# Performance work log

Measured on AMD Instinct MI355X. Metric: run time of the kernel, lower is better.

Reference implementation:

```python
import jax, jax.numpy as jnp
import numpy as np

NUM_STEPS = 151


def setup_inputs() -> dict:
    key = jax.random.key(0)
    k1, k2 = jax.random.split(key)
    feats = jax.random.normal(k1, (1024, 128), dtype=jnp.float32)
    # dists must lie in [-1, 1] -> L2-normalize embeddings (cosine similarity)
    feats = feats / jnp.linalg.norm(feats, axis=1, keepdims=True)
    classes = jax.random.randint(k2, (1024,), 0, 100, dtype=jnp.int32)
    return {"features": feats, "classes": classes}


def reference(features, classes):
    n = features.shape[0]
    step = 2.0 / (NUM_STEPS - 1)
    # bin centers t_j = -1 + j*step, j = 0..NUM_STEPS-1 (torch.range(-1, 1, step))
    t = (-1.0 + jnp.arange(NUM_STEPS, dtype=jnp.float32) * step)[:, None]  # [T,1]

    dists = features @ features.T                      # [N,N]
    iu = jnp.triu_indices(n, k=1)                      # strict upper triangle
    s = dists[iu]                                      # [P] pairwise similarities
    eq = (classes[:, None] == classes[None, :])[iu]    # [P] same-class mask

    pos_size = jnp.sum(eq).astype(jnp.float32)
    neg_size = jnp.sum(~eq).astype(jnp.float32)

    # snap each similarity to the bin edge below it (detached, like .data in torch)
    delta = jnp.floor((jax.lax.stop_gradient(s) + 1.0) / step) * step - 1.0  # [P]

    indsa = delta[None, :] == (t - step)   # s falls in [t-step, t): rising edge
    indsb = delta[None, :] == t            # s falls in [t, t+step): falling edge
    wa = (s[None, :] - t + step) / step
    wb = (-s[None, :] + t + step) / step
    w = jnp.where(indsa, wa, jnp.where(indsb, wb, 0.0))  # [T,P] triangular weights

    hist_pos = jnp.sum(jnp.where(eq[None, :], w, 0.0), axis=1) / pos_size  # [T]
    hist_neg = jnp.sum(jnp.where(eq[None, :], 0.0, w), axis=1) / neg_size  # [T]

    # tril(ones,-1) zeroing + sum over dim 0 == inclusive cumulative sum
    hist_pos_cdf = jnp.cumsum(hist_pos)
    loss = jnp.sum(hist_neg * hist_pos_cdf)
    return loss
```

## Files before the change

### kernel.cpp

```cpp
#include <hip/hip_runtime.h>

#define T_STEPS 151
#define NN 1024
#define DD 128
#define TILE 32
#define NTILE (NN / TILE)
#define NBLOCKS (NTILE * (NTILE + 1) / 2)
#define LDSTRIDE 132
#define NPAIRS 523776.0f


__global__ __launch_bounds__(256) void hist_kernel(
    const float* __restrict__ F, const int* __restrict__ cls, float* __restrict__ ws)
{
    __shared__ float As[TILE][LDSTRIDE];
    __shared__ float Bs[TILE][LDSTRIDE];
    __shared__ float hpos[T_STEPS];
    __shared__ float hneg[T_STEPS];
    __shared__ int   clsA[TILE];
    __shared__ int   clsB[TILE];
    __shared__ float pcount;

    const int t = threadIdx.x;

    int rem = blockIdx.x;
    int bi = 0;
    while (rem >= (NTILE - bi)) { rem -= (NTILE - bi); ++bi; }
    const int bj = bi + rem;

    for (int k = t; k < T_STEPS; k += 256) { hpos[k] = 0.f; hneg[k] = 0.f; }
    if (t == 0) pcount = 0.f;
    if (t < TILE)            clsA[t]        = cls[bi * TILE + t];
    else if (t < 2 * TILE)   clsB[t - TILE] = cls[bj * TILE + (t - TILE)];

    const float* Abase = F + (size_t)bi * TILE * DD;
    const float* Bbase = F + (size_t)bj * TILE * DD;
    for (int idx = t; idx < TILE * DD / 4; idx += 256) {
        int r = idx >> 5;
        int c = (idx & 31) << 2;
        *(float4*)&As[r][c] = *(const float4*)(Abase + r * DD + c);
        *(float4*)&Bs[r][c] = *(const float4*)(Bbase + r * DD + c);
    }
    __syncthreads();

    const int r  = t >> 5;
    const int c  = t & 31;
    const int gj = bj * TILE + c;
    const int cb = clsB[c];

    float acc[4][4];
    #pragma unroll
    for (int p = 0; p < 4; ++p)
        #pragma unroll
        for (int q = 0; q < 4; ++q) acc[p][q] = 0.f;

    #pragma unroll 4
    for (int k = 0; k < DD; k += 4) {
        float4 b4 = *(const float4*)&Bs[c][k];
        #pragma unroll
        for (int p = 0; p < 4; ++p) {
            float4 a4 = *(const float4*)&As[r + 8 * p][k];
            acc[p][0] += a4.x * b4.x;
            acc[p][1] += a4.y * b4.y;
            acc[p][2] += a4.z * b4.z;
            acc[p][3] += a4.w * b4.w;
        }
    }

    const float STEP = 2.0f / 150.0f;
    float myp = 0.f;
    {
        #pragma clang fp contract(off)
        #pragma unroll
        for (int p = 0; p < 4; ++p) {
            int i  = r + 8 * p;
            int gi = bi * TILE + i;
            if (gi < gj) {
                float s = (acc[p][0] + acc[p][1]) + (acc[p][2] + acc[p][3]);
                bool eqf = (clsA[i] == cb);
                float kf    = floorf((s + 1.0f) / STEP);
                float delta = kf * STEP - 1.0f;
                int   kk    = (int)kf;
                if (kk >= 0 && kk < T_STEPS) {
                    float tk = -1.0f + (float)kk * STEP;
                    if (delta == tk) {
                        float wb = (-s + tk + STEP) / STEP;
                        atomicAdd(eqf ? &hpos[kk] : &hneg[kk], wb);
                    }
                }
                int k1 = kk + 1;
                if (k1 >= 0 && k1 < T_STEPS) {
                    float tk1 = -1.0f + (float)k1 * STEP;
                    if (delta == (tk1 - STEP)) {
                        float wa = (s - tk1 + STEP) / STEP;
                        atomicAdd(eqf ? &hpos[k1] : &hneg[k1], wa);
                    }
                }
                if (eqf) myp += 1.f;
            }
        }
    }
    atomicAdd(&pcount, myp);
    __syncthreads();

    for (int k = t; k < T_STEPS; k += 256) {
        float hp = hpos[k], hn = hneg[k];
        if (hp != 0.f) atomicAdd(&ws[k], hp);
        if (hn != 0.f) atomicAdd(&ws[T_STEPS + k], hn);
    }
    if (t == 0) atomicAdd(&ws[2 * T_STEPS], pcount);
}

__global__ __launch_bounds__(192) void final_kernel(
    const float* __restrict__ ws, float* __restrict__ out)
{
    __shared__ float hp[T_STEPS], hn[T_STEPS];
    int t = threadIdx.x;
    float pos = ws[2 * T_STEPS];
    float neg = NPAIRS - pos;
    if (t < T_STEPS) {
        hp[t] = ws[t] / pos;
        hn[t] = ws[T_STEPS + t] / neg;
    }
    __syncthreads();
    if (t == 0) {
        #pragma clang fp contract(off)
        float cdf = 0.f, loss = 0.f;
        for (int j = 0; j < T_STEPS; ++j) { cdf += hp[j]; loss += hn[j] * cdf; }
        *out = loss;
    }
}

extern "C" void kernel_launch(void* const* d_in, const int* in_sizes, int n_in,
                              void* d_out, int out_size, void* d_ws, size_t ws_size,
                              hipStream_t stream)
{
    const float* F   = (const float*)d_in[0];
    const int*   cls = (const int*)d_in[1];
    float*       ws  = (float*)d_ws;
    float*       out = (float*)d_out;

    hipMemsetAsync(d_ws, 0, (2 * T_STEPS + 1) * sizeof(float), stream);
    hist_kernel<<<NBLOCKS, 256, 0, stream>>>(F, cls, ws);
    final_kernel<<<1, 192, 0, stream>>>(ws, out);
}
```

Before: 86.14 us.

## Use 2x2 register tiling and per-block partial histograms instead of global atomics

The dot-product loop changes from a 4x1 to a 2x2 register tile per thread, so each thread loads two A and two B float4 rows per k step and gets more reuse per LDS load. Each block now writes its full partial histogram and positive count to its own workspace row instead of doing global atomics. The final kernel reduces all 528 rows with 1024 threads, which also removes the memset launch. In exchange the final kernel reads about 640 KB of partials serially from one block, which may cost more than the global atomics did.

```diff
diff --git a/kernel.cpp b/kernel.cpp
--- a/kernel.cpp
+++ b/kernel.cpp
@@ -7,6 +7,7 @@
 #define NTILE (NN / TILE)
 #define NBLOCKS (NTILE * (NTILE + 1) / 2)
 #define LDSTRIDE 132
+#define WSROW 304
 #define NPAIRS 523776.0f
 
 
@@ -43,28 +44,31 @@
     }
     __syncthreads();
 
-    const int r  = t >> 5;
-    const int c  = t & 31;
-    const int gj = bj * TILE + c;
-    const int cb = clsB[c];
+    const int r2 = t >> 4;
+    const int c2 = t & 15;
 
-    float acc[4][4];
+    float acc[2][2][4];
     #pragma unroll
-    for (int p = 0; p < 4; ++p)
+    for (int a = 0; a < 2; ++a)
         #pragma unroll
-        for (int q = 0; q < 4; ++q) acc[p][q] = 0.f;
+        for (int b = 0; b < 2; ++b)
+            #pragma unroll
+            for (int q = 0; q < 4; ++q) acc[a][b][q] = 0.f;
 
     #pragma unroll 4
     for (int k = 0; k < DD; k += 4) {
-        float4 b4 = *(const float4*)&Bs[c][k];
-        #pragma unroll
-        for (int p = 0; p < 4; ++p) {
-            float4 a4 = *(const float4*)&As[r + 8 * p][k];
-            acc[p][0] += a4.x * b4.x;
-            acc[p][1] += a4.y * b4.y;
-            acc[p][2] += a4.z * b4.z;
-            acc[p][3] += a4.w * b4.w;
-        }
+        float4 a0 = *(const float4*)&As[r2][k];
+        float4 a1 = *(const float4*)&As[r2 + 16][k];
+        float4 b0 = *(const float4*)&Bs[c2][k];
+        float4 b1 = *(const float4*)&Bs[c2 + 16][k];
+        acc[0][0][0] += a0.x * b0.x; acc[0][0][1] += a0.y * b0.y;
+        acc[0][0][2] += a0.z * b0.z; acc[0][0][3] += a0.w * b0.w;
+        acc[0][1][0] += a0.x * b1.x; acc[0][1][1] += a0.y * b1.y;
+        acc[0][1][2] += a0.z * b1.z; acc[0][1][3] += a0.w * b1.w;
+        acc[1][0][0] += a1.x * b0.x; acc[1][0][1] += a1.y * b0.y;
+        acc[1][0][2] += a1.z * b0.z; acc[1][0][3] += a1.w * b0.w;
+        acc[1][1][0] += a1.x * b1.x; acc[1][1][1] += a1.y * b1.y;
+        acc[1][1][2] += a1.z * b1.z; acc[1][1][3] += a1.w * b1.w;
     }
 
     const float STEP = 2.0f / 150.0f;
@@ -72,61 +76,83 @@
     {
         #pragma clang fp contract(off)
         #pragma unroll
-        for (int p = 0; p < 4; ++p) {
-            int i  = r + 8 * p;
-            int gi = bi * TILE + i;
-            if (gi < gj) {
-                float s = (acc[p][0] + acc[p][1]) + (acc[p][2] + acc[p][3]);
-                bool eqf = (clsA[i] == cb);
-                float kf    = floorf((s + 1.0f) / STEP);
-                float delta = kf * STEP - 1.0f;
-                int   kk    = (int)kf;
-                if (kk >= 0 && kk < T_STEPS) {
-                    float tk = -1.0f + (float)kk * STEP;
-                    if (delta == tk) {
-                        float wb = (-s + tk + STEP) / STEP;
-                        atomicAdd(eqf ? &hpos[kk] : &hneg[kk], wb);
+        for (int ii = 0; ii < 2; ++ii) {
+            #pragma unroll
+            for (int jj = 0; jj < 2; ++jj) {
+                int gi = bi * TILE + r2 + 16 * ii;
+                int gj = bj * TILE + c2 + 16 * jj;
+                if (gi < gj) {
+                    float* a = acc[ii][jj];
+                    float s = (a[0] + a[1]) + (a[2] + a[3]);
+                    bool eqf = (clsA[r2 + 16 * ii] == clsB[c2 + 16 * jj]);
+                    float kf    = floorf((s + 1.0f) / STEP);
+                    float delta = kf * STEP - 1.0f;
+                    int   kk    = (int)kf;
+                    if (kk >= 0 && kk < T_STEPS) {
+                        float tk = -1.0f + (float)kk * STEP;
+                        if (delta == tk) {
+                            float wb = (-s + tk + STEP) / STEP;
+                            atomicAdd(eqf ? &hpos[kk] : &hneg[kk], wb);
+                        }
                     }
+                    int k1 = kk + 1;
+                    if (k1 >= 0 && k1 < T_STEPS) {
+                        float tk1 = -1.0f + (float)k1 * STEP;
+                        if (delta == (tk1 - STEP)) {
+                            float wa = (s - tk1 + STEP) / STEP;
+                            atomicAdd(eqf ? &hpos[k1] : &hneg[k1], wa);
+                        }
+                    }
+                    if (eqf) myp += 1.f;
                 }
-                int k1 = kk + 1;
-                if (k1 >= 0 && k1 < T_STEPS) {
-                    float tk1 = -1.0f + (float)k1 * STEP;
-                    if (delta == (tk1 - STEP)) {
-                        float wa = (s - tk1 + STEP) / STEP;
-                        atomicAdd(eqf ? &hpos[k1] : &hneg[k1], wa);
-                    }
-                }
-                if (eqf) myp += 1.f;
             }
         }
     }
     atomicAdd(&pcount, myp);
     __syncthreads();
 
-    for (int k = t; k < T_STEPS; k += 256) {
-        float hp = hpos[k], hn = hneg[k];
-        if (hp != 0.f) atomicAdd(&ws[k], hp);
-        if (hn != 0.f) atomicAdd(&ws[T_STEPS + k], hn);
+    float* base = ws + (size_t)blockIdx.x * WSROW;
+    for (int k = t; k < WSROW; k += 256) {
+        float v = (k < T_STEPS)     ? hpos[k]
+                : (k < 2 * T_STEPS) ? hneg[k - T_STEPS]
+                : (k == 2 * T_STEPS)? pcount : 0.f;
+        base[k] = v;
     }
-    if (t == 0) atomicAdd(&ws[2 * T_STEPS], pcount);
 }
 
-__global__ __launch_bounds__(192) void final_kernel(
+__global__ __launch_bounds__(1024) void final_kernel(
     const float* __restrict__ ws, float* __restrict__ out)
 {
+    __shared__ float part[3][WSROW];
     __shared__ float hp[T_STEPS], hn[T_STEPS];
-    int t = threadIdx.x;
-    float pos = ws[2 * T_STEPS];
-    float neg = NPAIRS - pos;
-    if (t < T_STEPS) {
-        hp[t] = ws[t] / pos;
-        hn[t] = ws[T_STEPS + t] / neg;
+    __shared__ float poss;
+    const int t = threadIdx.x;
+
+    if (t < 3 * WSROW) {
+        const int j = t % WSROW;
+        const int g = t / WSROW;
+        float s = 0.f;
+        #pragma unroll 4
+        for (int b = g; b < NBLOCKS; b += 3) s += ws[(size_t)b * WSROW + j];
+        part[g][j] = s;
+    }
+    __syncthreads();
+    if (t < WSROW) {
+        float v = part[0][t] + part[1][t] + part[2][t];
+        if (t < T_STEPS)            hp[t] = v;
+        else if (t < 2 * T_STEPS)   hn[t - T_STEPS] = v;
+        else if (t == 2 * T_STEPS)  poss = v;
     }
     __syncthreads();
     if (t == 0) {
         #pragma clang fp contract(off)
+        float pos = poss;
+        float neg = NPAIRS - pos;
         float cdf = 0.f, loss = 0.f;
-        for (int j = 0; j < T_STEPS; ++j) { cdf += hp[j]; loss += hn[j] * cdf; }
+        for (int j = 0; j < T_STEPS; ++j) {
+            cdf  += hp[j] / pos;
+            loss += (hn[j] / neg) * cdf;
+        }
         *out = loss;
     }
 }
@@ -140,7 +166,6 @@
     float*       ws  = (float*)d_ws;
     float*       out = (float*)d_out;
 
-    hipMemsetAsync(d_ws, 0, (2 * T_STEPS + 1) * sizeof(float), stream);
     hist_kernel<<<NBLOCKS, 256, 0, stream>>>(F, cls, ws);
-    final_kernel<<<1, 192, 0, stream>>>(ws, out);
+    final_kernel<<<1, 1024, 0, stream>>>(ws, out);
 }
```

Result: slower. 93.60 us (+8.7%).
